# Optimization experiments

Hardware: AMD Instinct MI355X
Metric: run time of the kernel (lower is better)

## Reference

```python
import jax, jax.numpy as jnp
import numpy as np

EMBED_DIM = 512
NUM_HEADS = 8
NUM_RULES = 16
HEAD_DIM = EMBED_DIM // NUM_HEADS


def setup_inputs() -> dict:
    key = jax.random.key(0)
    ks = jax.random.split(key, 10)
    B, S, E, H, R, D = 4, 2048, EMBED_DIM, NUM_HEADS, NUM_RULES, HEAD_DIM
    lim_q = 1.0 / np.sqrt(E)
    lim_v = 1.0 / np.sqrt(E)
    return {
        "query": jax.random.normal(ks[0], (B, S, E), jnp.float32),
        "key": jax.random.normal(ks[1], (B, S, E), jnp.float32),
        "value": jax.random.normal(ks[2], (B, S, E), jnp.float32),
        "Wq": jax.random.uniform(ks[3], (E, E), jnp.float32, -lim_q, lim_q),
        "bq": jax.random.uniform(ks[4], (E,), jnp.float32, -lim_q, lim_q),
        "Wv": jax.random.uniform(ks[5], (E * R, E), jnp.float32, -lim_v, lim_v),
        "bv": jax.random.uniform(ks[6], (E * R,), jnp.float32, -lim_v, lim_v),
        "Wo": jax.random.uniform(ks[7], (E, E), jnp.float32, -lim_q, lim_q),
        "bo": jax.random.uniform(ks[8], (E,), jnp.float32, -lim_q, lim_q),
        "rules_keys": 0.02 * jax.random.normal(ks[9], (H, R, D), jnp.float32),
        "rules_widths": jnp.ones((H, R, D), jnp.float32),
    }


def reference(query, key, value, Wq, bq, Wv, bv, Wo, bo, rules_keys, rules_widths):
    B, S, E = query.shape
    H, R, D = NUM_HEADS, NUM_RULES, HEAD_DIM
    scale = D ** -0.5
    # preprocessing_query: Linear + scale, split heads -> (b, h, s, d)
    q = (query @ Wq.T + bq) * scale
    q = q.reshape(B, S, H, D).transpose(0, 2, 1, 3)
    # custom_distance (l1): |q - rule_key| broadcast over rules -> (b, h, s, r, d)
    diff = jnp.abs(q[:, :, :, None, :] - rules_keys[None, :, None, :, :])
    # get_z_values: z = mean_d( -0.5 * (diff / width)^2 ) -> (b, h, s, r)
    z = -0.5 * jnp.mean(jnp.square(diff / rules_widths[None, :, None, :, :]), axis=-1)
    # softmax over rules (last dim), dropout is identity (p=0)
    attn = jax.nn.softmax(z, axis=-1)  # (b, h, s, r)
    # preprocessing_value: Linear(E -> E*R) + scale, 'b s (h d r) -> b s h d r'
    v = (value @ Wv.T + bv) * scale
    v = v.reshape(B, S, H, D, R)
    # Fnn_output = attn * v summed over rules -> (b, s, h, d)
    out = jnp.einsum("bhsr,bshdr->bshd", attn, v)
    # torch: (b,s,h,d).transpose(1,2).contiguous().view(b, -1, h*d)
    out = out.transpose(0, 2, 1, 3).reshape(B, -1, H * D)
    return out @ Wo.T + bo
```

## Files before the change

kernel.cpp:

```cpp
#include <hip/hip_runtime.h>
#include <stdint.h>

#define TOKENS 8192
#define EDIM 512
#define HNUM 8
#define RNUM 16
#define DDIM 64
#define KDIM 512

typedef short v8s __attribute__((ext_vector_type(8)));
typedef float v4f __attribute__((ext_vector_type(4)));

__device__ inline float b2f(unsigned short u) {
    union { unsigned int i; float f; } c; c.i = ((unsigned int)u) << 16; return c.f;
}
__device__ inline unsigned short f2b(float f) {
    union { float f; unsigned int i; } c; c.f = f;
    unsigned int i = c.i + 0x7fffu + ((c.i >> 16) & 1u);
    return (unsigned short)(i >> 16);
}

#define GLD16(dst, src) \
    __builtin_amdgcn_global_load_lds((__attribute__((address_space(1))) void*)(src), \
                                     (__attribute__((address_space(3))) void*)(dst), 16, 0, 0)

__global__ __launch_bounds__(256)
void cvt5(const float* __restrict__ s0, const float* __restrict__ s1,
          const float* __restrict__ s2, const float* __restrict__ s3,
          const float* __restrict__ s4,
          unsigned short* __restrict__ d0, unsigned short* __restrict__ d1,
          unsigned short* __restrict__ d2, unsigned short* __restrict__ d3,
          unsigned short* __restrict__ d4,
          int n0, int n1, int n2, int n3, int n4)
{
    const float* s; unsigned short* d; int n;
    switch (blockIdx.y) {
        case 0: s = s0; d = d0; n = n0; break;
        case 1: s = s1; d = d1; n = n1; break;
        case 2: s = s2; d = d2; n = n2; break;
        case 3: s = s3; d = d3; n = n3; break;
        default: s = s4; d = d4; n = n4; break;
    }
    size_t base = (size_t)blockIdx.x * 2048 + (size_t)threadIdx.x * 8;
    if (base >= (size_t)n) return;
    const float4* sp = (const float4*)(s + base);
    float4 f0 = sp[0], f1 = sp[1];
    v8s o;
    o[0] = (short)f2b(f0.x); o[1] = (short)f2b(f0.y);
    o[2] = (short)f2b(f0.z); o[3] = (short)f2b(f0.w);
    o[4] = (short)f2b(f1.x); o[5] = (short)f2b(f1.y);
    o[6] = (short)f2b(f1.z); o[7] = (short)f2b(f1.w);
    *(v8s*)(d + base) = o;
}

template <int MODE>
__global__ __launch_bounds__(256, 4)
void gemm64(const unsigned short* __restrict__ A,
            const unsigned short* __restrict__ B,
            const float* __restrict__ bias,
            float* __restrict__ outF,
            unsigned short* __restrict__ outH)
{
    __shared__ unsigned short As[64 * 32];
    __shared__ unsigned short Bs[64 * 32];

    const int tid  = threadIdx.x;
    const int w    = tid >> 6;
    const int lane = tid & 63;
    const int quad = lane >> 4;
    const int l16  = lane & 15;
    const int wm   = w >> 1, wn = w & 1;
    const int m0   = blockIdx.x * 64;
    const int n0   = blockIdx.y * 64;

    v4f acc[2][2];
#pragma unroll
    for (int i = 0; i < 2; ++i)
#pragma unroll
        for (int j = 0; j < 2; ++j)
            acc[i][j] = (v4f){0.f, 0.f, 0.f, 0.f};

    for (int kt = 0; kt < KDIM / 32; ++kt) {
        int c = w * 64 + lane;
        const unsigned short* sa = A + (size_t)(m0 + (c >> 2)) * KDIM + kt * 32 + (c & 3) * 8;
        GLD16(&As[w * 512], sa);
        const unsigned short* sb = B + (size_t)(n0 + (c >> 2)) * KDIM + kt * 32 + (c & 3) * 8;
        GLD16(&Bs[w * 512], sb);
        __syncthreads();

        v8s af[2], bf[2];
#pragma unroll
        for (int mt = 0; mt < 2; ++mt)
            af[mt] = *(const v8s*)&As[(wm * 32 + mt * 16 + l16) * 32 + quad * 8];
#pragma unroll
        for (int nt = 0; nt < 2; ++nt)
            bf[nt] = *(const v8s*)&Bs[(wn * 32 + nt * 16 + l16) * 32 + quad * 8];
#pragma unroll
        for (int mt = 0; mt < 2; ++mt)
#pragma unroll
            for (int nt = 0; nt < 2; ++nt)
                acc[mt][nt] = __builtin_amdgcn_mfma_f32_16x16x32_bf16(af[mt], bf[nt], acc[mt][nt], 0, 0, 0);
        __syncthreads();
    }

#pragma unroll
    for (int mt = 0; mt < 2; ++mt)
#pragma unroll
        for (int nt = 0; nt < 2; ++nt) {
            int col = n0 + wn * 32 + nt * 16 + l16;
            float bb = bias[col];
#pragma unroll
            for (int rg = 0; rg < 4; ++rg) {
                int row = m0 + wm * 32 + mt * 16 + quad * 4 + rg;
                float v = acc[mt][nt][rg] + bb;
                if (MODE == 0) outH[(size_t)row * EDIM + col] = f2b(v * 0.125f);
                else           outF[(size_t)row * EDIM + col] = v;
            }
        }
}

__device__ __forceinline__ v8s ldfrag(const unsigned short* base, int r, int g) {
    return *(const v8s*)(base + (r << 6) + ((g ^ (r & 7)) << 3));
}

#define SCHED0 __builtin_amdgcn_sched_barrier(0)
#define BARX do { SCHED0; __builtin_amdgcn_s_barrier(); SCHED0; } while (0)
#define LGKM0 do { asm volatile("s_waitcnt lgkmcnt(0)" ::: "memory"); SCHED0; } while (0)
#define WAITV(n) do { asm volatile("s_waitcnt vmcnt(" #n ")" ::: "memory"); SCHED0; } while (0)

#define STAGE_H(ldsArr, bufi, half_, gptr, rowbase, ktv) do { \
    const unsigned short* s_ = (gptr) + (size_t)((rowbase) + (half_) * 128 + (w << 4) + rsub) * KDIM \
                               + (ktv) * 64 + (gsw << 3); \
    GLD16(&ldsArr[bufi][(half_) * 8192 + (w << 10)], s_); \
    GLD16(&ldsArr[bufi][(half_) * 8192 + (w << 10) + 512], s_ + 8 * KDIM); \
} while (0)

#define LDA8(mq_) do { \
    _Pragma("unroll") \
    for (int mi = 0; mi < 4; ++mi) \
        _Pragma("unroll") \
        for (int ks = 0; ks < 2; ++ks) \
            af[mi * 2 + ks] = ldfrag(abase, wm * 64 + (mq_) * 128 + mi * 16 + l16, ks * 4 + quad); \
} while (0)

#define LDB4(nq_) do { \
    _Pragma("unroll") \
    for (int ni = 0; ni < 2; ++ni) \
        _Pragma("unroll") \
        for (int ks = 0; ks < 2; ++ks) \
            bf[ni * 2 + ks] = ldfrag(bbase, wn * 32 + (nq_) * 128 + ni * 16 + l16, ks * 4 + quad); \
} while (0)

#define MFMA16(mq_, nq_) do { \
    _Pragma("unroll") \
    for (int ks = 0; ks < 2; ++ks) \
        _Pragma("unroll") \
        for (int mi = 0; mi < 4; ++mi) \
            _Pragma("unroll") \
            for (int ni = 0; ni < 2; ++ni) \
                acc[(mq_) * 2 + (nq_)][mi][ni] = __builtin_amdgcn_mfma_f32_16x16x32_bf16( \
                    af[mi * 2 + ks], bf[ni * 2 + ks], acc[(mq_) * 2 + (nq_)][mi][ni], 0, 0, 0); \
} while (0)

__global__ __launch_bounds__(512, 2)
void gemm_v(const unsigned short* __restrict__ A,
            const unsigned short* __restrict__ B,
            const float* __restrict__ bias,
            unsigned short* __restrict__ outH,
            const float* __restrict__ attn)
{
    __shared__ unsigned short As[2][16384];
    __shared__ unsigned short Bs[2][16384];

    const int tid  = threadIdx.x;
    const int w    = tid >> 6;
    const int lane = tid & 63;
    const int quad = lane >> 4;
    const int l16  = lane & 15;
    const int wm   = w >> 2;
    const int wn   = w & 3;
    const int rsub = lane >> 3;
    const int gsw  = (lane & 7) ^ rsub;

    const int id = ((blockIdx.x & 7) << 7) | (blockIdx.x >> 3);
    const int m0 = (id & 31) << 8;
    const int n0 = (id >> 5) << 8;

    v4f acc[4][4][2];
#pragma unroll
    for (int q = 0; q < 4; ++q)
#pragma unroll
        for (int mi = 0; mi < 4; ++mi)
#pragma unroll
            for (int ni = 0; ni < 2; ++ni)
                acc[q][mi][ni] = (v4f){0.f, 0.f, 0.f, 0.f};

    v8s af[8], bf[4];

    STAGE_H(As, 0, 0, A, m0, 0);
    STAGE_H(Bs, 0, 1, B, n0, 0);
    STAGE_H(As, 0, 1, A, m0, 0);
    STAGE_H(Bs, 0, 0, B, n0, 0);
    STAGE_H(As, 1, 0, A, m0, 1);
    STAGE_H(Bs, 1, 1, B, n0, 1);
    WAITV(4);
    BARX;

    for (int T = 0; T < KDIM / 64; ++T) {
        const unsigned short* abase = &As[T & 1][0];
        const unsigned short* bbase = &Bs[T & 1][0];
        const int bn_ = (T & 1) ^ 1;

        LDA8(0); LDB4(0);
        if (T + 1 < 8) STAGE_H(As, bn_, 1, A, m0, T + 1);
        BARX; LGKM0;
        __builtin_amdgcn_s_setprio(1); MFMA16(0, 0); __builtin_amdgcn_s_setprio(0);
        BARX;

        LDB4(1);
        if (T + 1 < 8) STAGE_H(Bs, bn_, 0, B, n0, T + 1);
        BARX; LGKM0;
        __builtin_amdgcn_s_setprio(1); MFMA16(0, 1); __builtin_amdgcn_s_setprio(0);
        BARX;

        LDA8(1);
        if (T + 2 < 8) STAGE_H(As, T & 1, 0, A, m0, T + 2);
        BARX; LGKM0;
        __builtin_amdgcn_s_setprio(1); MFMA16(1, 1); __builtin_amdgcn_s_setprio(0);
        BARX;

        LDB4(0);
        if (T + 2 < 8) STAGE_H(Bs, T & 1, 1, B, n0, T + 2);
        BARX; LGKM0;
        __builtin_amdgcn_s_setprio(1); MFMA16(1, 0); __builtin_amdgcn_s_setprio(0);
        if (T < 6) { WAITV(4); } else { WAITV(0); }
        BARX;
    }

    unsigned short* Osp = &As[0][0];
    const int h  = m0 >> 10;
    const int d0 = (m0 >> 4) & 63;
#pragma unroll
    for (int mq = 0; mq < 2; ++mq)
#pragma unroll
        for (int nq = 0; nq < 2; ++nq)
#pragma unroll
            for (int mi = 0; mi < 4; ++mi) {
                float4 bias4 = *(const float4*)&bias[m0 + mq * 128 + wm * 64 + mi * 16 + quad * 4];
#pragma unroll
                for (int ni = 0; ni < 2; ++ni) {
                    int tloc  = nq * 128 + wn * 32 + ni * 16 + l16;
                    float4 av = *(const float4*)&attn[(size_t)(n0 + tloc) * (HNUM * RNUM) + h * RNUM + quad * 4];
                    v4f a = acc[mq * 2 + nq][mi][ni];
                    float val = (a[0] + bias4.x) * av.x + (a[1] + bias4.y) * av.y
                              + (a[2] + bias4.z) * av.z + (a[3] + bias4.w) * av.w;
                    val += __shfl_xor(val, 16);
                    val += __shfl_xor(val, 32);
                    if (quad == 0)
                        Osp[tloc * 16 + (mq * 8 + wm * 4 + mi)] = f2b(val * 0.125f);
                }
            }
    __syncthreads();
    {
        int tl = tid >> 1, hf = tid & 1;
        int sg = n0 + tl;
        int g  = (sg >> 11) * 2048 + h * 256 + ((sg & 2047) >> 3);
        int j  = (sg & 7) * 64 + d0 + hf * 8;
        *(v8s*)&outH[(size_t)g * EDIM + j] = *(const v8s*)&Osp[tl * 16 + hf * 8];
    }
}

#define RST 72
__global__ __launch_bounds__(256)
void rules_softmax(const unsigned short* __restrict__ q,
                   const float* __restrict__ rk,
                   const float* __restrict__ rw,
                   float* __restrict__ attn)
{
    __shared__ float ql[16 * RST];
    __shared__ float rkl[16 * RST];
    __shared__ float iwl[16 * RST];
    const int h   = blockIdx.y;
    const int t0  = blockIdx.x * 16;
    const int tid = threadIdx.x;

#pragma unroll
    for (int i = 0; i < 4; ++i) {
        int jj = tid + i * 256;
        int r = jj >> 6, d = jj & 63;
        rkl[r * RST + d] = rk[h * (RNUM * DDIM) + jj];
        float wv = rw[h * (RNUM * DDIM) + jj];
        iwl[r * RST + d] = 1.0f / (wv * wv);
    }
    {
        int jj = tid * 4;
        int row = jj >> 6, d = jj & 63;
        const unsigned short* src = q + (size_t)(t0 + row) * EDIM + h * DDIM + d;
        unsigned short u0 = src[0], u1 = src[1], u2 = src[2], u3 = src[3];
        ql[row * RST + d + 0] = b2f(u0);
        ql[row * RST + d + 1] = b2f(u1);
        ql[row * RST + d + 2] = b2f(u2);
        ql[row * RST + d + 3] = b2f(u3);
    }
    __syncthreads();

    const int tl = tid >> 4;
    const int r  = tid & 15;
    const float* qrow = &ql[tl * RST];
    const float* krow = &rkl[r * RST];
    const float* wrow = &iwl[r * RST];
    float z = 0.f;
#pragma unroll
    for (int d4 = 0; d4 < 16; ++d4) {
        float4 qv = *(const float4*)&qrow[d4 * 4];
        float4 kv = *(const float4*)&krow[d4 * 4];
        float4 wv = *(const float4*)&wrow[d4 * 4];
        float a0 = qv.x - kv.x; z += a0 * a0 * wv.x;
        float a1 = qv.y - kv.y; z += a1 * a1 * wv.y;
        float a2 = qv.z - kv.z; z += a2 * a2 * wv.z;
        float a3 = qv.w - kv.w; z += a3 * a3 * wv.w;
    }
    z *= (-0.5f / 64.f);
    float mx = z;
#pragma unroll
    for (int s = 1; s < 16; s <<= 1) mx = fmaxf(mx, __shfl_xor(mx, s));
    float e = __expf(z - mx);
    float sum = e;
#pragma unroll
    for (int s = 1; s < 16; s <<= 1) sum += __shfl_xor(sum, s);
    attn[(size_t)(t0 + tl) * (HNUM * RNUM) + h * RNUM + r] = e / sum;
}

extern "C" void kernel_launch(void* const* d_in, const int* in_sizes, int n_in,
                              void* d_out, int out_size, void* d_ws, size_t ws_size,
                              hipStream_t stream) {
    const float* query = (const float*)d_in[0];
    const float* value = (const float*)d_in[2];
    const float* Wq = (const float*)d_in[3];
    const float* bq = (const float*)d_in[4];
    const float* Wv = (const float*)d_in[5];
    const float* bv = (const float*)d_in[6];
    const float* Wo = (const float*)d_in[7];
    const float* bo = (const float*)d_in[8];
    const float* rk = (const float*)d_in[9];
    const float* rw = (const float*)d_in[10];

    char* ws = (char*)d_ws;
    unsigned short* qbf  = (unsigned short*)(ws);
    unsigned short* vbf  = (unsigned short*)(ws + (size_t)( 8 << 20));
    unsigned short* Wqb  = (unsigned short*)(ws + (size_t)(16 << 20));
    unsigned short* Wvb  = (unsigned short*)(ws + (size_t)(17 << 20));
    unsigned short* Wob  = (unsigned short*)(ws + (size_t)(25 << 20));
    unsigned short* out1 = (unsigned short*)(ws + (size_t)(26 << 20));
    unsigned short* qf   = (unsigned short*)(ws + (size_t)(34 << 20));
    float* attn          = (float*)(ws + (size_t)(42 << 20));

    dim3 blk(256);
    cvt5<<<dim3(2048, 5), blk, 0, stream>>>(query, value, Wv, Wq, Wo,
                                            qbf, vbf, Wvb, Wqb, Wob,
                                            TOKENS * EDIM, TOKENS * EDIM, EDIM * RNUM * EDIM,
                                            EDIM * EDIM, EDIM * EDIM);
    gemm64<0><<<dim3(TOKENS / 64, EDIM / 64), blk, 0, stream>>>(qbf, Wqb, bq, nullptr, qf);
    rules_softmax<<<dim3(TOKENS / 16, HNUM), blk, 0, stream>>>(qf, rk, rw, attn);
    gemm_v<<<dim3(1024), dim3(512), 0, stream>>>(Wvb, vbf, bv, out1, attn);
    gemm64<2><<<dim3(TOKENS / 64, EDIM / 64), blk, 0, stream>>>(out1, Wob, bo, (float*)d_out, nullptr);
}
```

Measured before the change: 245.2 us.

## Keep both B fragments in registers, remap block tiles, drop sched barriers in gemm_v

```diff
diff --git a/kernel.cpp b/kernel.cpp
--- a/kernel.cpp
+++ b/kernel.cpp
@@ -123,10 +123,9 @@
     return *(const v8s*)(base + (r << 6) + ((g ^ (r & 7)) << 3));
 }
 
-#define SCHED0 __builtin_amdgcn_sched_barrier(0)
-#define BARX do { SCHED0; __builtin_amdgcn_s_barrier(); SCHED0; } while (0)
-#define LGKM0 do { asm volatile("s_waitcnt lgkmcnt(0)" ::: "memory"); SCHED0; } while (0)
-#define WAITV(n) do { asm volatile("s_waitcnt vmcnt(" #n ")" ::: "memory"); SCHED0; } while (0)
+#define BAR   __builtin_amdgcn_s_barrier()
+#define LGKM0 asm volatile("s_waitcnt lgkmcnt(0)" ::: "memory")
+#define WAITV(n) asm volatile("s_waitcnt vmcnt(" #n ")" ::: "memory")
 
 #define STAGE_H(ldsArr, bufi, half_, gptr, rowbase, ktv) do { \
     const unsigned short* s_ = (gptr) + (size_t)((rowbase) + (half_) * 128 + (w << 4) + rsub) * KDIM \
@@ -143,23 +142,23 @@
             af[mi * 2 + ks] = ldfrag(abase, wm * 64 + (mq_) * 128 + mi * 16 + l16, ks * 4 + quad); \
 } while (0)
 
-#define LDB4(nq_) do { \
+#define LDB4(nq_, dst) do { \
     _Pragma("unroll") \
     for (int ni = 0; ni < 2; ++ni) \
         _Pragma("unroll") \
         for (int ks = 0; ks < 2; ++ks) \
-            bf[ni * 2 + ks] = ldfrag(bbase, wn * 32 + (nq_) * 128 + ni * 16 + l16, ks * 4 + quad); \
+            dst[ni * 2 + ks] = ldfrag(bbase, wn * 32 + (nq_) * 128 + ni * 16 + l16, ks * 4 + quad); \
 } while (0)
 
-#define MFMA16(mq_, nq_) do { \
+#define MFMA16(ai_, bfr) do { \
     _Pragma("unroll") \
     for (int ks = 0; ks < 2; ++ks) \
         _Pragma("unroll") \
         for (int mi = 0; mi < 4; ++mi) \
             _Pragma("unroll") \
             for (int ni = 0; ni < 2; ++ni) \
-                acc[(mq_) * 2 + (nq_)][mi][ni] = __builtin_amdgcn_mfma_f32_16x16x32_bf16( \
-                    af[mi * 2 + ks], bf[ni * 2 + ks], acc[(mq_) * 2 + (nq_)][mi][ni], 0, 0, 0); \
+                acc[ai_][mi][ni] = __builtin_amdgcn_mfma_f32_16x16x32_bf16( \
+                    af[mi * 2 + ks], bfr[ni * 2 + ks], acc[ai_][mi][ni], 0, 0, 0); \
 } while (0)
 
 __global__ __launch_bounds__(512, 2)
@@ -182,9 +181,12 @@
     const int rsub = lane >> 3;
     const int gsw  = (lane & 7) ^ rsub;
 
-    const int id = ((blockIdx.x & 7) << 7) | (blockIdx.x >> 3);
-    const int m0 = (id & 31) << 8;
-    const int n0 = (id >> 5) << 8;
+    const int c  = blockIdx.x & 7;
+    const int j  = blockIdx.x >> 3;
+    const int mb = (j & 7) | ((j >> 5) << 3);
+    const int nb = (j >> 3) & 3;
+    const int m0 = mb << 8;
+    const int n0 = (c * 4 + nb) << 8;
 
     v4f acc[4][4][2];
 #pragma unroll
@@ -195,46 +197,46 @@
             for (int ni = 0; ni < 2; ++ni)
                 acc[q][mi][ni] = (v4f){0.f, 0.f, 0.f, 0.f};
 
-    v8s af[8], bf[4];
+    v8s af[8], bf0[4], bf1[4];
 
     STAGE_H(As, 0, 0, A, m0, 0);
+    STAGE_H(Bs, 0, 0, B, n0, 0);
+    STAGE_H(As, 0, 1, A, m0, 0);
     STAGE_H(Bs, 0, 1, B, n0, 0);
-    STAGE_H(As, 0, 1, A, m0, 0);
-    STAGE_H(Bs, 0, 0, B, n0, 0);
     STAGE_H(As, 1, 0, A, m0, 1);
     STAGE_H(Bs, 1, 1, B, n0, 1);
     WAITV(4);
-    BARX;
-
+    BAR;
+
+#pragma unroll
     for (int T = 0; T < KDIM / 64; ++T) {
         const unsigned short* abase = &As[T & 1][0];
         const unsigned short* bbase = &Bs[T & 1][0];
         const int bn_ = (T & 1) ^ 1;
 
-        LDA8(0); LDB4(0);
+        LDA8(0); LDB4(0, bf0);
         if (T + 1 < 8) STAGE_H(As, bn_, 1, A, m0, T + 1);
-        BARX; LGKM0;
-        __builtin_amdgcn_s_setprio(1); MFMA16(0, 0); __builtin_amdgcn_s_setprio(0);
-        BARX;
-
-        LDB4(1);
+        BAR; LGKM0;
+        __builtin_amdgcn_s_setprio(1); MFMA16(0, bf0); __builtin_amdgcn_s_setprio(0);
+        BAR;
+
+        LDB4(1, bf1);
         if (T + 1 < 8) STAGE_H(Bs, bn_, 0, B, n0, T + 1);
-        BARX; LGKM0;
-        __builtin_amdgcn_s_setprio(1); MFMA16(0, 1); __builtin_amdgcn_s_setprio(0);
-        BARX;
+        BAR; LGKM0;
+        __builtin_amdgcn_s_setprio(1); MFMA16(1, bf1); __builtin_amdgcn_s_setprio(0);
+        BAR;
 
         LDA8(1);
         if (T + 2 < 8) STAGE_H(As, T & 1, 0, A, m0, T + 2);
-        BARX; LGKM0;
-        __builtin_amdgcn_s_setprio(1); MFMA16(1, 1); __builtin_amdgcn_s_setprio(0);
-        BARX;
-
-        LDB4(0);
+        BAR; LGKM0;
+        __builtin_amdgcn_s_setprio(1); MFMA16(3, bf1); __builtin_amdgcn_s_setprio(0);
+        BAR;
+
         if (T + 2 < 8) STAGE_H(Bs, T & 1, 1, B, n0, T + 2);
-        BARX; LGKM0;
-        __builtin_amdgcn_s_setprio(1); MFMA16(1, 0); __builtin_amdgcn_s_setprio(0);
+        BAR; LGKM0;
+        __builtin_amdgcn_s_setprio(1); MFMA16(2, bf0); __builtin_amdgcn_s_setprio(0);
         if (T < 6) { WAITV(4); } else { WAITV(0); }
-        BARX;
+        BAR;
     }
 
     unsigned short* Osp = &As[0][0];
@@ -265,8 +267,8 @@
         int tl = tid >> 1, hf = tid & 1;
         int sg = n0 + tl;
         int g  = (sg >> 11) * 2048 + h * 256 + ((sg & 2047) >> 3);
-        int j  = (sg & 7) * 64 + d0 + hf * 8;
-        *(v8s*)&outH[(size_t)g * EDIM + j] = *(const v8s*)&Osp[tl * 16 + hf * 8];
+        int jx = (sg & 7) * 64 + d0 + hf * 8;
+        *(v8s*)&outH[(size_t)g * EDIM + jx] = *(const v8s*)&Osp[tl * 16 + hf * 8];
     }
 }
 
```

After: 230.0 us. -6.2%, faster.
